# Kernel tuning notes

Measured on AMD Instinct MI355X. Metric: run time of the kernel, lower is better.

The kernel has to match this reference:

```python
import jax, jax.numpy as jnp
import numpy as np

N_NODES = 1_000_000
BATCH = 100_000
DIM_NIG = 128
DIM_NODE = 128


def setup_inputs() -> dict:
    key = jax.random.key(0)
    ks = jax.random.split(key, 9)
    return {
        "src_node_ids": jax.random.randint(ks[0], (BATCH,), 0, N_NODES),
        "dst_node_ids": jax.random.randint(ks[1], (BATCH,), 0, N_NODES),
        "previous_embedding": jax.random.normal(ks[2], (N_NODES, DIM_NODE), jnp.float32),
        "batch_src_neighbor_embedding": jax.random.normal(ks[3], (BATCH, DIM_NIG), jnp.float32),
        "batch_dst_neighbor_embedding": jax.random.normal(ks[4], (BATCH, DIM_NIG), jnp.float32),
        # neighbor_layer: Linear(dim_nig -> dim_node); torch weight layout [out, in]
        "W_nig": jax.random.normal(ks[5], (DIM_NODE, DIM_NIG), jnp.float32) / np.sqrt(DIM_NIG),
        "b_nig": jax.random.normal(ks[6], (DIM_NODE,), jnp.float32) * 0.01,
        # node_layer: Linear(dim_node -> dim_node)
        "W_node": jax.random.normal(ks[7], (DIM_NODE, DIM_NODE), jnp.float32) / np.sqrt(DIM_NODE),
        "b_node": jax.random.normal(ks[8], (DIM_NODE,), jnp.float32) * 0.01,
    }


def _update(prev_emb, node_ids, nbr_emb, W_nig, b_nig, W_node, b_node):
    prev = jnp.take(prev_emb, node_ids, axis=0)          # [B, D] gather
    shift = nbr_emb @ W_nig.T + b_nig                    # [B, D]
    return (prev + shift) @ W_node.T + b_node + prev     # linear + residual


def reference(src_node_ids, dst_node_ids, previous_embedding,
              batch_src_neighbor_embedding, batch_dst_neighbor_embedding,
              W_nig, b_nig, W_node, b_node):
    src_emb = _update(previous_embedding, src_node_ids, batch_src_neighbor_embedding,
                      W_nig, b_nig, W_node, b_node)
    dst_emb = _update(previous_embedding, dst_node_ids, batch_dst_neighbor_embedding,
                      W_nig, b_nig, W_node, b_node)
    # clone().detach() in torch -> stop_gradient base, then scatter src then dst
    updated = jax.lax.stop_gradient(previous_embedding)
    updated = updated.at[src_node_ids].set(src_emb)
    updated = updated.at[dst_node_ids].set(dst_emb)
    return updated
```

## Files before the change

kernel.cpp:

```cpp
#include <hip/hip_runtime.h>
#include <hip/hip_bf16.h>

#define B_SZ 100000
#define NTOT 200000
#define NN   1000000
#define DIM  128

typedef short bf16x8 __attribute__((ext_vector_type(8)));
typedef float f32x4  __attribute__((ext_vector_type(4)));

__device__ __forceinline__ short f2bf(float f) {
    union { float f; unsigned u; } v; v.f = f;
    unsigned u = v.u;
    u += 0x7fffu + ((u >> 16) & 1u);
    return (short)(u >> 16);
}

__global__ void k_init(int* __restrict__ owner) {
    int i = blockIdx.x * 256 + threadIdx.x;
    if (i < NN) owner[i] = -1;
}

__global__ void k_claim(const int* __restrict__ src, const int* __restrict__ dst,
                        int* __restrict__ owner) {
    int i = blockIdx.x * 256 + threadIdx.x;
    if (i >= NTOT) return;
    int node = (i < B_SZ) ? src[i] : dst[i - B_SZ];
    atomicMax(&owner[node], i);
}

__global__ void k_weights(const float* __restrict__ Wnig, const float* __restrict__ bnig,
                          const float* __restrict__ Wnode, const float* __restrict__ bnode,
                          short* __restrict__ PA, short* __restrict__ PQ,
                          float* __restrict__ cvec) {
    int b = blockIdx.x, t = threadIdx.x;
    if (b < 32) {
        int kc = b >> 3, nc = b & 7;
        int n = nc * 16 + (t & 15);
        int kbase = kc * 32 + (t >> 4) * 8;
        int fo = (b * 64 + t) * 8;
        for (int i = 0; i < 8; ++i) {
            int k = kbase + i;
            float a = Wnode[n * DIM + k] + (k == n ? 1.0f : 0.0f);
            PA[fo + i] = f2bf(a);
            float q = 0.f;
            for (int m = 0; m < DIM; ++m) q += Wnode[n * DIM + m] * Wnig[m * DIM + k];
            PQ[fo + i] = f2bf(q);
        }
    } else {
        for (int j = t; j < DIM; j += 64) {
            float c = bnode[j];
            for (int k = 0; k < DIM; ++k) c += bnig[k] * Wnode[j * DIM + k];
            cvec[j] = c;
        }
    }
}

__global__ __launch_bounds__(256) void k_main(
        const int* __restrict__ src, const int* __restrict__ dst,
        const float* __restrict__ prev,
        const float* __restrict__ nsrc, const float* __restrict__ ndst,
        const int* __restrict__ owner,
        const short* __restrict__ PA, const short* __restrict__ PQ,
        const float* __restrict__ cvec,
        float* __restrict__ out) {
    int wave = threadIdx.x >> 6;
    int lane = threadIdx.x & 63;
    int rowbase = (blockIdx.x * 4 + wave) * 16;

    int arow = rowbase + (lane & 15);
    bool is_src = arow < B_SZ;
    int bi = is_src ? arow : arow - B_SZ;
    const int* ids = is_src ? src : dst;
    const float* nbr = is_src ? nsrc : ndst;
    int node_a = ids[bi];
    const float* prow = prev + (long)node_a * DIM;
    const float* nrow = nbr + (long)bi * DIM;
    int koff = (lane >> 4) * 8;

    f32x4 acc[8];
#pragma unroll
    for (int nc = 0; nc < 8; ++nc) acc[nc] = (f32x4){0.f, 0.f, 0.f, 0.f};

#pragma unroll
    for (int kc = 0; kc < 4; ++kc) {
        int k0 = kc * 32 + koff;
        float4 p0 = *(const float4*)(prow + k0);
        float4 p1 = *(const float4*)(prow + k0 + 4);
        float4 n0 = *(const float4*)(nrow + k0);
        float4 n1 = *(const float4*)(nrow + k0 + 4);
        bf16x8 aP, aN;
        aP[0] = f2bf(p0.x); aP[1] = f2bf(p0.y); aP[2] = f2bf(p0.z); aP[3] = f2bf(p0.w);
        aP[4] = f2bf(p1.x); aP[5] = f2bf(p1.y); aP[6] = f2bf(p1.z); aP[7] = f2bf(p1.w);
        aN[0] = f2bf(n0.x); aN[1] = f2bf(n0.y); aN[2] = f2bf(n0.z); aN[3] = f2bf(n0.w);
        aN[4] = f2bf(n1.x); aN[5] = f2bf(n1.y); aN[6] = f2bf(n1.z); aN[7] = f2bf(n1.w);
#pragma unroll
        for (int nc = 0; nc < 8; ++nc) {
            int fo = ((kc * 8 + nc) * 64 + lane) * 8;
            bf16x8 bA = *(const bf16x8*)(PA + fo);
            bf16x8 bQ = *(const bf16x8*)(PQ + fo);
            acc[nc] = __builtin_amdgcn_mfma_f32_16x16x32_bf16(aP, bA, acc[nc], 0, 0, 0);
            acc[nc] = __builtin_amdgcn_mfma_f32_16x16x32_bf16(aN, bQ, acc[nc], 0, 0, 0);
        }
    }

    int col0 = lane & 15;
    float cv[8];
#pragma unroll
    for (int nc = 0; nc < 8; ++nc) cv[nc] = cvec[nc * 16 + col0];

#pragma unroll
    for (int r = 0; r < 4; ++r) {
        int row = rowbase + (lane >> 4) * 4 + r;
        bool s = row < B_SZ;
        int b2 = s ? row : row - B_SZ;
        int node = (s ? src : dst)[b2];
        if (owner[node] == row) {
            float* orow = out + (long)node * DIM;
#pragma unroll
            for (int nc = 0; nc < 8; ++nc) {
                orow[nc * 16 + col0] = acc[nc][r] + cv[nc];
            }
        }
    }
}

__global__ void k_copy(const float* __restrict__ prev, const int* __restrict__ owner,
                       float* __restrict__ out) {
    long t = (long)blockIdx.x * blockDim.x + threadIdx.x;
    long stride = (long)gridDim.x * blockDim.x;
    const long total = (long)NN * 32;
    for (; t < total; t += stride) {
        int row = (int)(t >> 5);
        if (owner[row] < 0) {
            int c = (int)(t & 31);
            float4 v = ((const float4*)prev)[(long)row * 32 + c];
            ((float4*)out)[(long)row * 32 + c] = v;
        }
    }
}

extern "C" void kernel_launch(void* const* d_in, const int* in_sizes, int n_in,
                              void* d_out, int out_size, void* d_ws, size_t ws_size,
                              hipStream_t stream) {
    const int*   src  = (const int*)d_in[0];
    const int*   dst  = (const int*)d_in[1];
    const float* prev = (const float*)d_in[2];
    const float* nsrc = (const float*)d_in[3];
    const float* ndst = (const float*)d_in[4];
    const float* Wnig = (const float*)d_in[5];
    const float* bnig = (const float*)d_in[6];
    const float* Wnode = (const float*)d_in[7];
    const float* bnode = (const float*)d_in[8];
    float* out = (float*)d_out;

    const size_t OWNER_B = (size_t)NN * 4;
    const size_t PA_B = 32 * 64 * 8 * 2;
    if (ws_size < OWNER_B + 2 * PA_B + 512) return;
    char* ws = (char*)d_ws;
    int*   owner = (int*)ws;
    short* PA = (short*)(ws + OWNER_B);
    short* PQ = (short*)(ws + OWNER_B + PA_B);
    float* cvec = (float*)(ws + OWNER_B + 2 * PA_B);

    k_init<<<(NN + 255) / 256, 256, 0, stream>>>(owner);
    k_claim<<<(NTOT + 255) / 256, 256, 0, stream>>>(src, dst, owner);
    k_weights<<<33, 64, 0, stream>>>(Wnig, bnig, Wnode, bnode, PA, PQ, cvec);
    k_main<<<3125, 256, 0, stream>>>(src, dst, prev, nsrc, ndst, owner, PA, PQ, cvec, out);
    k_copy<<<2048, 256, 0, stream>>>(prev, owner, out);
}
```

Measured before the change: 291.0 us.

## Merge init with weight prep and copy with main into combined launches

Folds the owner-array init and the weight-fragment precompute into one launch, with the weight work spread over 256-thread blocks. The copy of untouched rows and the MFMA update of the batch rows become one launch split by block index, so the two independent phases run at once on the GPU. This cuts two kernel launches and lets the bandwidth-bound copy overlap the gather/MFMA work. The price is a larger grid whose copy blocks are dispatched first.

```diff
diff --git a/kernel.cpp b/kernel.cpp
--- a/kernel.cpp
+++ b/kernel.cpp
@@ -5,6 +5,12 @@
 #define NTOT 200000
 #define NN   1000000
 #define DIM  128
+
+#define NB_INIT   3907
+#define NB_WFRAG  32
+#define NB_CLAIM  782
+#define NB_COPY   2048
+#define NB_MAIN   3125
 
 typedef short bf16x8 __attribute__((ext_vector_type(8)));
 typedef float f32x4  __attribute__((ext_vector_type(4)));
@@ -16,9 +22,39 @@
     return (short)(u >> 16);
 }
 
-__global__ void k_init(int* __restrict__ owner) {
-    int i = blockIdx.x * 256 + threadIdx.x;
-    if (i < NN) owner[i] = -1;
+__global__ __launch_bounds__(256) void k_init_weights(
+        int* __restrict__ owner,
+        const float* __restrict__ Wnig, const float* __restrict__ bnig,
+        const float* __restrict__ Wnode, const float* __restrict__ bnode,
+        short* __restrict__ PA, short* __restrict__ PQ,
+        float* __restrict__ cvec) {
+    int b = blockIdx.x, t = threadIdx.x;
+    if (b < NB_INIT) {
+        int i = b * 256 + t;
+        if (i < NN) owner[i] = -1;
+    } else if (b < NB_INIT + NB_WFRAG) {
+        int b2 = b - NB_INIT;
+        int lane = t & 63, ig = t >> 6;
+        int kc = b2 >> 3, nc = b2 & 7;
+        int n = nc * 16 + (lane & 15);
+        int kbase = kc * 32 + (lane >> 4) * 8;
+        int fo = (b2 * 64 + lane) * 8;
+        for (int ii = 0; ii < 2; ++ii) {
+            int i = ig * 2 + ii;
+            int k = kbase + i;
+            float a = Wnode[n * DIM + k] + (k == n ? 1.0f : 0.0f);
+            PA[fo + i] = f2bf(a);
+            float q = 0.f;
+            for (int m = 0; m < DIM; ++m) q += Wnode[n * DIM + m] * Wnig[m * DIM + k];
+            PQ[fo + i] = f2bf(q);
+        }
+    } else {
+        if (t < DIM) {
+            float c = bnode[t];
+            for (int k = 0; k < DIM; ++k) c += bnig[k] * Wnode[t * DIM + k];
+            cvec[t] = c;
+        }
+    }
 }
 
 __global__ void k_claim(const int* __restrict__ src, const int* __restrict__ dst,
@@ -29,34 +65,7 @@
     atomicMax(&owner[node], i);
 }
 
-__global__ void k_weights(const float* __restrict__ Wnig, const float* __restrict__ bnig,
-                          const float* __restrict__ Wnode, const float* __restrict__ bnode,
-                          short* __restrict__ PA, short* __restrict__ PQ,
-                          float* __restrict__ cvec) {
-    int b = blockIdx.x, t = threadIdx.x;
-    if (b < 32) {
-        int kc = b >> 3, nc = b & 7;
-        int n = nc * 16 + (t & 15);
-        int kbase = kc * 32 + (t >> 4) * 8;
-        int fo = (b * 64 + t) * 8;
-        for (int i = 0; i < 8; ++i) {
-            int k = kbase + i;
-            float a = Wnode[n * DIM + k] + (k == n ? 1.0f : 0.0f);
-            PA[fo + i] = f2bf(a);
-            float q = 0.f;
-            for (int m = 0; m < DIM; ++m) q += Wnode[n * DIM + m] * Wnig[m * DIM + k];
-            PQ[fo + i] = f2bf(q);
-        }
-    } else {
-        for (int j = t; j < DIM; j += 64) {
-            float c = bnode[j];
-            for (int k = 0; k < DIM; ++k) c += bnig[k] * Wnode[j * DIM + k];
-            cvec[j] = c;
-        }
-    }
-}
-
-__global__ __launch_bounds__(256) void k_main(
+__global__ __launch_bounds__(256) void k_fused(
         const int* __restrict__ src, const int* __restrict__ dst,
         const float* __restrict__ prev,
         const float* __restrict__ nsrc, const float* __restrict__ ndst,
@@ -64,9 +73,25 @@
         const short* __restrict__ PA, const short* __restrict__ PQ,
         const float* __restrict__ cvec,
         float* __restrict__ out) {
+    if (blockIdx.x < NB_COPY) {
+        long t = (long)blockIdx.x * 256 + threadIdx.x;
+        const long stride = (long)NB_COPY * 256;
+        const long total = (long)NN * 32;
+        for (; t < total; t += stride) {
+            int row = (int)(t >> 5);
+            if (owner[row] < 0) {
+                int c = (int)(t & 31);
+                float4 v = ((const float4*)prev)[(long)row * 32 + c];
+                ((float4*)out)[(long)row * 32 + c] = v;
+            }
+        }
+        return;
+    }
+
+    int bid = blockIdx.x - NB_COPY;
     int wave = threadIdx.x >> 6;
     int lane = threadIdx.x & 63;
-    int rowbase = (blockIdx.x * 4 + wave) * 16;
+    int rowbase = (bid * 4 + wave) * 16;
 
     int arow = rowbase + (lane & 15);
     bool is_src = arow < B_SZ;
@@ -125,21 +150,6 @@
     }
 }
 
-__global__ void k_copy(const float* __restrict__ prev, const int* __restrict__ owner,
-                       float* __restrict__ out) {
-    long t = (long)blockIdx.x * blockDim.x + threadIdx.x;
-    long stride = (long)gridDim.x * blockDim.x;
-    const long total = (long)NN * 32;
-    for (; t < total; t += stride) {
-        int row = (int)(t >> 5);
-        if (owner[row] < 0) {
-            int c = (int)(t & 31);
-            float4 v = ((const float4*)prev)[(long)row * 32 + c];
-            ((float4*)out)[(long)row * 32 + c] = v;
-        }
-    }
-}
-
 extern "C" void kernel_launch(void* const* d_in, const int* in_sizes, int n_in,
                               void* d_out, int out_size, void* d_ws, size_t ws_size,
                               hipStream_t stream) {
@@ -163,9 +173,9 @@
     short* PQ = (short*)(ws + OWNER_B + PA_B);
     float* cvec = (float*)(ws + OWNER_B + 2 * PA_B);
 
-    k_init<<<(NN + 255) / 256, 256, 0, stream>>>(owner);
-    k_claim<<<(NTOT + 255) / 256, 256, 0, stream>>>(src, dst, owner);
-    k_weights<<<33, 64, 0, stream>>>(Wnig, bnig, Wnode, bnode, PA, PQ, cvec);
-    k_main<<<3125, 256, 0, stream>>>(src, dst, prev, nsrc, ndst, owner, PA, PQ, cvec, out);
-    k_copy<<<2048, 256, 0, stream>>>(prev, owner, out);
+    k_init_weights<<<NB_INIT + NB_WFRAG + 1, 256, 0, stream>>>(
+        owner, Wnig, bnig, Wnode, bnode, PA, PQ, cvec);
+    k_claim<<<NB_CLAIM, 256, 0, stream>>>(src, dst, owner);
+    k_fused<<<NB_COPY + NB_MAIN, 256, 0, stream>>>(
+        src, dst, prev, nsrc, ndst, owner, PA, PQ, cvec, out);
 }
```

After: 352.6 us. 1.21x slower.
